# Kernel optimization log

Measured on AMD Instinct MI355X. Metric: run time of the kernel, lower is better.

Reference implementation:

```python
import jax, jax.numpy as jnp
import numpy as np

H, DH, BS = 12, 64, 64          # heads, head_dim, block_size
D, FF, L, EPS = 768, 3072, 12, 1e-12

def _ln(x, g, b):
    m = x.mean(-1, keepdims=True)
    v = ((x - m) ** 2).mean(-1, keepdims=True)
    return (x - m) * jax.lax.rsqrt(v + EPS) * g + b

def setup_inputs() -> dict:
    key = jax.random.key(0)
    ks = iter(jax.random.split(key, 40))
    B, S, IN, C = 2, 4096, 1280, 2
    nb = S // BS
    def p(shape, s=0.02):
        return jax.random.normal(next(ks), shape, jnp.float32) * s
    inp = dict(
        embeddings=jax.random.normal(next(ks), (B, S, IN), jnp.float32),
        attention_mask=jnp.ones((B, S), jnp.int32),
        Wp=p((IN, D)), bp=jnp.zeros((D,), jnp.float32),
        pos_emb=p((S, D)), tok_emb=p((D,)),
        lne_g=jnp.ones((D,), jnp.float32), lne_b=jnp.zeros((D,), jnp.float32),
        Wq=p((L, D, D)), bq=jnp.zeros((L, D), jnp.float32),
        Wk=p((L, D, D)), bk=jnp.zeros((L, D), jnp.float32),
        Wv=p((L, D, D)), bv=jnp.zeros((L, D), jnp.float32),
        Wo=p((L, D, D)), bo=jnp.zeros((L, D), jnp.float32),
        l1g=jnp.ones((L, D), jnp.float32), l1b=jnp.zeros((L, D), jnp.float32),
        W1=p((L, D, FF)), b1=jnp.zeros((L, FF), jnp.float32),
        W2=p((L, FF, D)), b2=jnp.zeros((L, D), jnp.float32),
        l2g=jnp.ones((L, D), jnp.float32), l2b=jnp.zeros((L, D), jnp.float32),
        Wc=p((D, C)), bc=jnp.zeros((C,), jnp.float32),
    )
    # BigBird pattern: each interior query block -> 2 global + 3 window + 3 random key blocks.
    # Random blocks are drawn once (deterministic) like HF's data-independent rand mask.
    rng = np.random.default_rng(0)
    idx, val = [], []
    for i in range(1, nb - 1):
        blocks = [0, nb - 1, i - 1, i, i + 1]
        v = [True, True, i - 1 != 0, True, i + 1 != nb - 1]  # dedupe window/global overlap
        forbid = set(blocks)
        allowed = [x for x in range(nb) if x not in forbid]
        r = rng.choice(allowed, size=3, replace=False).tolist()
        idx.append(blocks + r)
        val.append(v + [True, True, True])
    inp["blk_idx"] = jnp.asarray(np.array(idx, np.int32))    # [nb-2, 8]
    inp["blk_valid"] = jnp.asarray(np.array(val, bool))       # [nb-2, 8]
    return inp

def reference(embeddings, attention_mask, Wp, bp, pos_emb, tok_emb, lne_g, lne_b,
              Wq, bq, Wk, bk, Wv, bv, Wo, bo, l1g, l1b, W1, b1, W2, b2, l2g, l2b,
              Wc, bc, blk_idx, blk_valid):
    B, S, _ = embeddings.shape
    nb = S // BS
    na = blk_idx.shape[1]
    x = embeddings @ Wp + bp + pos_emb + tok_emb
    x = _ln(x, lne_g, lne_b)
    am = attention_mask.astype(jnp.float32)                       # [B,S]
    full_bias = ((am - 1.0) * 1e9)[:, None, None, None, :]        # [B,1,1,1,S]
    amb = am.reshape(B, nb, BS)
    am_g = amb[:, blk_idx].reshape(B, nb - 2, na * BS)            # gathered key mask
    vmask = jnp.repeat(blk_valid, BS, axis=-1)                    # [nb-2, na*BS]
    gb = jnp.where((am_g > 0) & vmask[None], 0.0, -1e9)[:, None, :, None, :]
    scale = 1.0 / np.sqrt(DH).astype(np.float32)

    def layer(x, p):
        wq, bq_, wk, bk_, wv, bv_, wo, bo_, g1, b1_, w1, bi1, w2, bi2, g2, b2_ = p
        q = (x @ wq + bq_).reshape(B, S, H, DH).transpose(0, 2, 1, 3)
        k = (x @ wk + bk_).reshape(B, S, H, DH).transpose(0, 2, 1, 3)
        v = (x @ wv + bv_).reshape(B, S, H, DH).transpose(0, 2, 1, 3)
        qb = q.reshape(B, H, nb, BS, DH)
        kb = k.reshape(B, H, nb, BS, DH)
        vb = v.reshape(B, H, nb, BS, DH)
        # interior query blocks: gather sparse key blocks (global+window+random)
        q_int = qb[:, :, 1:-1]                                     # [B,H,nb-2,BS,DH]
        k_g = kb[:, :, blk_idx].reshape(B, H, nb - 2, na * BS, DH)
        v_g = vb[:, :, blk_idx].reshape(B, H, nb - 2, na * BS, DH)
        s = jnp.einsum('bhiqd,bhikd->bhiqk', q_int, k_g) * scale + gb
        p_ = jax.nn.softmax(s, axis=-1)
        ctx_int = jnp.einsum('bhiqk,bhikd->bhiqd', p_, v_g)
        # first/last blocks are global: attend to all keys
        q_edge = jnp.stack([qb[:, :, 0], qb[:, :, -1]], axis=2)    # [B,H,2,BS,DH]
        se = jnp.einsum('bheqd,bhkd->bheqk', q_edge, k) * scale + full_bias
        pe = jax.nn.softmax(se, axis=-1)
        ctx_e = jnp.einsum('bheqk,bhkd->bheqd', pe, v)
        ctx = jnp.concatenate([ctx_e[:, :, :1], ctx_int, ctx_e[:, :, 1:]], axis=2)
        ctx = ctx.reshape(B, H, S, DH).transpose(0, 2, 1, 3).reshape(B, S, D)
        x = _ln(x + ctx @ wo + bo_, g1, b1_)
        h = jax.nn.gelu(x @ w1 + bi1, approximate=False) @ w2 + bi2
        x = _ln(x + h, g2, b2_)
        return x, None

    x, _ = jax.lax.scan(layer, x, (Wq, bq, Wk, bk, Wv, bv, Wo, bo,
                                   l1g, l1b, W1, b1, W2, b2, l2g, l2b))
    return x[:, 0, :] @ Wc + bc
```

## Files before the change

kernel.cpp:

```cpp
#include <hip/hip_runtime.h>
#include <hip/hip_bf16.h>
#include <math.h>

using bf16 = __hip_bfloat16;
typedef short bf16x8 __attribute__((ext_vector_type(8)));
typedef float f32x4 __attribute__((ext_vector_type(4)));

#define DEV __device__ __forceinline__

constexpr int BATCH = 2, SEQ = 4096, INPD = 1280, DM = 768, FFD = 3072;
constexpr int NL = 12, NH = 12, DHD = 64, NBLK = 64, NCLS = 2;
constexpr int MR = BATCH * SEQ;
constexpr int QKVN = 3 * DM;
constexpr int NJOBS = 62 + 16;
constexpr int PARTF = 64 * 64 + 128;

DEV void gload_lds16(const void* g, void* l) {
  __builtin_amdgcn_global_load_lds(
      (const __attribute__((address_space(1))) unsigned int*)g,
      (__attribute__((address_space(3))) unsigned int*)l, 16, 0, 0);
}

__global__ void k_f32_to_bf16(const float* __restrict__ in, bf16* __restrict__ out, int n) {
  int i = (blockIdx.x * blockDim.x + threadIdx.x) * 4;
  int stride = gridDim.x * blockDim.x * 4;
  for (; i < n; i += stride) {
    float4 v = *(const float4*)(in + i);
    out[i + 0] = __float2bfloat16(v.x);
    out[i + 1] = __float2bfloat16(v.y);
    out[i + 2] = __float2bfloat16(v.z);
    out[i + 3] = __float2bfloat16(v.w);
  }
}

DEV void tr32_tile(const float* __restrict__ src, bf16* __restrict__ dst,
                   int K, int N, int tile, float t[32][33], int tid) {
  int nt = N >> 5;
  int tk = tile / nt, tn = tile - tk * nt;
  int tx = tid & 31, ty = tid >> 5;
#pragma unroll
  for (int i = 0; i < 4; ++i)
    t[ty + 8 * i][tx] = src[(size_t)(tk * 32 + ty + 8 * i) * N + tn * 32 + tx];
  __syncthreads();
#pragma unroll
  for (int i = 0; i < 4; ++i)
    dst[(size_t)(tn * 32 + ty + 8 * i) * K + tk * 32 + tx] = __float2bfloat16(t[tx][ty + 8 * i]);
}

__global__ __launch_bounds__(256) void k_transpose_one(const float* __restrict__ src,
                                                       bf16* __restrict__ dst, int K, int N) {
  __shared__ float t[32][33];
  tr32_tile(src, dst, K, N, blockIdx.x, t, threadIdx.x);
}

__global__ __launch_bounds__(256) void k_transpose_layer(
    const float* __restrict__ Wq, const float* __restrict__ Wk,
    const float* __restrict__ Wv, const float* __restrict__ Wo,
    const float* __restrict__ W1, const float* __restrict__ W2,
    bf16* __restrict__ wqkvT, bf16* __restrict__ woT,
    bf16* __restrict__ w1T, bf16* __restrict__ w2T, int l) {
  __shared__ float t[32][33];
  int id = blockIdx.x;
  const float* src; bf16* dst; int K, N;
  if (id < 1728) {
    int m = id / 576; id -= m * 576;
    src = (m == 0 ? Wq : m == 1 ? Wk : Wv) + (size_t)l * DM * DM;
    dst = wqkvT + (size_t)m * DM * DM; K = DM; N = DM;
  } else if (id < 2304) {
    id -= 1728; src = Wo + (size_t)l * DM * DM; dst = woT; K = DM; N = DM;
  } else if (id < 4608) {
    id -= 2304; src = W1 + (size_t)l * DM * FFD; dst = w1T; K = DM; N = FFD;
  } else {
    id -= 4608; src = W2 + (size_t)l * FFD * DM; dst = w2T; K = FFD; N = DM;
  }
  tr32_tile(src, dst, K, N, id, t, threadIdx.x);
}

template <int EPI>
__global__ __launch_bounds__(256) void k_gemm(
    const bf16* __restrict__ A, const bf16* __restrict__ BT, int N, int K,
    const float* __restrict__ b0, const float* __restrict__ b1, const float* __restrict__ b2,
    const float* __restrict__ res, const float* __restrict__ pos, const float* __restrict__ tok,
    float* __restrict__ Cf, bf16* __restrict__ Cb) {
  __shared__ __align__(16) bf16 lA[128 * 32];
  __shared__ __align__(16) bf16 lB[128 * 32];
  const int tid = threadIdx.x;
  const int bm = blockIdx.y * 128, bn = blockIdx.x * 128;
  const int lane = tid & 63, wid = tid >> 6;
  const int wm = (wid >> 1) * 64, wn = (wid & 1) * 64;
  const int lr = lane & 15, lks = lane >> 4;
  f32x4 acc[4][4] = {};
  for (int k0 = 0; k0 < K; k0 += 32) {
    __syncthreads();
#pragma unroll
    for (int ss = 0; ss < 2; ++ss) {
      int seg = tid + ss * 256;
      int row = seg >> 2, slot = seg & 3;
      int kseg = slot ^ ((row >> 1) & 3);
      gload_lds16(A + (size_t)(bm + row) * K + k0 + kseg * 8, lA + seg * 8);
      gload_lds16(BT + (size_t)(bn + row) * K + k0 + kseg * 8, lB + seg * 8);
    }
    __syncthreads();
    bf16x8 af[4], bfr[4];
#pragma unroll
    for (int m = 0; m < 4; ++m) {
      int r = wm + m * 16 + lr;
      af[m] = *(const bf16x8*)(lA + r * 32 + ((lks ^ ((r >> 1) & 3)) << 3));
    }
#pragma unroll
    for (int n = 0; n < 4; ++n) {
      int r = wn + n * 16 + lr;
      bfr[n] = *(const bf16x8*)(lB + r * 32 + ((lks ^ ((r >> 1) & 3)) << 3));
    }
#pragma unroll
    for (int m = 0; m < 4; ++m)
#pragma unroll
      for (int n = 0; n < 4; ++n)
        acc[m][n] = __builtin_amdgcn_mfma_f32_16x16x32_bf16(af[m], bfr[n], acc[m][n], 0, 0, 0);
  }
  const int gq = lane >> 4;
#pragma unroll
  for (int m = 0; m < 4; ++m) {
#pragma unroll
    for (int n = 0; n < 4; ++n) {
      int gcol = bn + wn + n * 16 + lr;
      f32x4 v = acc[m][n];
#pragma unroll
      for (int r = 0; r < 4; ++r) {
        int grow = bm + wm + m * 16 + gq * 4 + r;
        float x = v[r];
        if constexpr (EPI == 0) {
          int c = gcol; const float* bb = b0;
          if (c >= 2 * DM) { bb = b2; c -= 2 * DM; }
          else if (c >= DM) { bb = b1; c -= DM; }
          x += bb[c];
          Cb[(size_t)grow * N + gcol] = __float2bfloat16(x);
        } else if constexpr (EPI == 1) {
          x += b0[gcol];
          x = 0.5f * x * (1.0f + erff(x * 0.70710678118654752f));
          Cb[(size_t)grow * N + gcol] = __float2bfloat16(x);
        } else if constexpr (EPI == 2) {
          x += b0[gcol] + res[(size_t)grow * N + gcol];
          Cf[(size_t)grow * N + gcol] = x;
        } else {
          x += b0[gcol] + pos[(size_t)(grow & (SEQ - 1)) * N + gcol] + tok[gcol];
          Cf[(size_t)grow * N + gcol] = x;
        }
      }
    }
  }
}

__global__ __launch_bounds__(256) void k_ln(const float* __restrict__ in,
                                            const float* __restrict__ g, const float* __restrict__ b,
                                            float* __restrict__ xf, bf16* __restrict__ xb) {
  const int row = blockIdx.x, tid = threadIdx.x;
  const float* rp = in + (size_t)row * DM;
  float vals[3], s = 0.f, s2 = 0.f;
#pragma unroll
  for (int i = 0; i < 3; ++i) {
    float v = rp[tid + i * 256];
    vals[i] = v; s += v; s2 += v * v;
  }
#pragma unroll
  for (int off = 32; off > 0; off >>= 1) {
    s += __shfl_down(s, off);
    s2 += __shfl_down(s2, off);
  }
  __shared__ float red[8];
  int wv = tid >> 6, lane = tid & 63;
  if (lane == 0) { red[wv] = s; red[4 + wv] = s2; }
  __syncthreads();
  s = red[0] + red[1] + red[2] + red[3];
  s2 = red[4] + red[5] + red[6] + red[7];
  float mean = s * (1.0f / DM);
  float var = s2 * (1.0f / DM) - mean * mean;
  float rs = rsqrtf(var + 1e-12f);
#pragma unroll
  for (int i = 0; i < 3; ++i) {
    int c = tid + i * 256;
    float y = (vals[i] - mean) * rs * g[c] + b[c];
    xf[(size_t)row * DM + c] = y;
    xb[(size_t)row * DM + c] = __float2bfloat16(y);
  }
}

__global__ __launch_bounds__(256) void k_vt(const bf16* __restrict__ qkv, bf16* __restrict__ vt) {
  __shared__ unsigned short t[64][72];
  const int bh = blockIdx.y, t0 = blockIdx.x * 64;
  const int b = bh / NH, h = bh - b * NH;
  const int tid = threadIdx.x;
  const int rr = tid >> 2, cs = (tid & 3) * 16;
  const unsigned short* src = (const unsigned short*)qkv +
      (size_t)(b * SEQ + t0 + rr) * QKVN + 2 * DM + h * DHD + cs;
#pragma unroll
  for (int i = 0; i < 16; ++i) t[cs + i][rr] = src[i];
  __syncthreads();
  unsigned short* dst = (unsigned short*)vt + (size_t)(bh * DHD + rr) * SEQ + t0 + cs;
#pragma unroll
  for (int i = 0; i < 16; ++i) dst[i] = t[rr][cs + i];
}

__global__ __launch_bounds__(256) void k_attn(
    const bf16* __restrict__ qkv, const bf16* __restrict__ vt,
    const int* __restrict__ blk_idx,
    bf16* __restrict__ ctx, float* __restrict__ epart) {
  __shared__ __align__(16) bf16 sQ[64 * 64];
  __shared__ __align__(16) bf16 sK[64 * 64];
  __shared__ __align__(16) bf16 sV[64 * 64];
  __shared__ __align__(16) bf16 sP[4][16 * 64];
  const int job = blockIdx.x;
  const int b = job / (NH * NJOBS);
  const int rem = job - b * NH * NJOBS;
  const int h = rem / NJOBS;
  const int j = rem - h * NJOBS;
  const int tid = threadIdx.x, lane = tid & 63, w = tid >> 6;
  const int lr = lane & 15, lks = lane >> 4;

  const bool interior = (j < 62);
  int qblk, e = 0, split = 0;
  if (interior) qblk = j + 1;
  else { int tt = j - 62; e = tt >> 3; split = tt & 7; qblk = e ? NBLK - 1 : 0; }
  const int qt0 = qblk * 64;

  {
    const bf16* qbase = qkv + (size_t)(b * SEQ + qt0) * QKVN + h * DHD;
#pragma unroll
    for (int ss = 0; ss < 2; ++ss) {
      int seg = tid + ss * 256;
      int row = seg >> 3, slot = seg & 7;
      int kseg = slot ^ (row & 7);
      gload_lds16(qbase + (size_t)row * QKVN + kseg * 8, sQ + seg * 8);
    }
  }
  __syncthreads();
  bf16x8 aq[2];
#pragma unroll
  for (int kk = 0; kk < 2; ++kk) {
    int rq = w * 16 + lr;
    int slot = (kk * 4 + lks) ^ (rq & 7);
    aq[kk] = *(const bf16x8*)(sQ + rq * 64 + slot * 8);
  }

  float m_r[4], l_r[4];
  f32x4 o[4] = {};
#pragma unroll
  for (int r = 0; r < 4; ++r) { m_r[r] = -1e30f; l_r[r] = 0.f; }

  for (int kb = 0; kb < 8; ++kb) {
    int kbi;
    if (interior) {
      if ((j == 0 && kb == 2) || (j == 61 && kb == 4)) continue;
      kbi = blk_idx[j * 8 + kb];
    } else {
      kbi = split * 8 + kb;
    }
    const int kt0 = kbi * 64;
    __syncthreads();
    {
      const bf16* kbase = qkv + (size_t)(b * SEQ + kt0) * QKVN + DM + h * DHD;
      const bf16* vbase = vt + (size_t)((b * NH + h) * DHD) * SEQ + kt0;
#pragma unroll
      for (int ss = 0; ss < 2; ++ss) {
        int seg = tid + ss * 256;
        int row = seg >> 3, slot = seg & 7;
        int kseg = slot ^ (row & 7);
        gload_lds16(kbase + (size_t)row * QKVN + kseg * 8, sK + seg * 8);
        gload_lds16(vbase + (size_t)row * SEQ + kseg * 8, sV + seg * 8);
      }
    }
    __syncthreads();
    f32x4 sfr[4];
#pragma unroll
    for (int n = 0; n < 4; ++n) {
      f32x4 z = {};
#pragma unroll
      for (int kk = 0; kk < 2; ++kk) {
        int rk = n * 16 + lr;
        int slot = (kk * 4 + lks) ^ (rk & 7);
        bf16x8 kf = *(const bf16x8*)(sK + rk * 64 + slot * 8);
        z = __builtin_amdgcn_mfma_f32_16x16x32_bf16(aq[kk], kf, z, 0, 0, 0);
      }
      sfr[n] = z;
    }
#pragma unroll
    for (int n = 0; n < 4; ++n)
#pragma unroll
      for (int r = 0; r < 4; ++r) sfr[n][r] *= 0.125f;
    float alpha[4];
#pragma unroll
    for (int r = 0; r < 4; ++r) {
      float tmx = fmaxf(fmaxf(sfr[0][r], sfr[1][r]), fmaxf(sfr[2][r], sfr[3][r]));
#pragma unroll
      for (int off = 1; off < 16; off <<= 1) tmx = fmaxf(tmx, __shfl_xor(tmx, off));
      float mnew = fmaxf(m_r[r], tmx);
      alpha[r] = __expf(m_r[r] - mnew);
      m_r[r] = mnew;
    }
#pragma unroll
    for (int r = 0; r < 4; ++r) {
      float su = 0.f;
#pragma unroll
      for (int n = 0; n < 4; ++n) {
        float p = __expf(sfr[n][r] - m_r[r]);
        sfr[n][r] = p;
        su += p;
      }
#pragma unroll
      for (int off = 1; off < 16; off <<= 1) su += __shfl_xor(su, off);
      l_r[r] = l_r[r] * alpha[r] + su;
    }
#pragma unroll
    for (int n = 0; n < 4; ++n) {
#pragma unroll
      for (int r = 0; r < 4; ++r) {
        int prow = lks * 4 + r;
        int col = n * 16 + lr;
        int eo = prow * 64 + ((((col >> 3) ^ (prow & 7)) << 3) | (col & 7));
        sP[w][eo] = __float2bfloat16(sfr[n][r]);
      }
    }
#pragma unroll
    for (int n = 0; n < 4; ++n)
#pragma unroll
      for (int r = 0; r < 4; ++r) o[n][r] *= alpha[r];
    asm volatile("s_waitcnt lgkmcnt(0)" ::: "memory");
    bf16x8 pa[2];
#pragma unroll
    for (int kk = 0; kk < 2; ++kk) {
      int slot = (kk * 4 + lks) ^ (lr & 7);
      pa[kk] = *(const bf16x8*)(sP[w] + lr * 64 + slot * 8);
    }
#pragma unroll
    for (int n = 0; n < 4; ++n) {
#pragma unroll
      for (int kk = 0; kk < 2; ++kk) {
        int rv = n * 16 + lr;
        int slot = (kk * 4 + lks) ^ (rv & 7);
        bf16x8 vf = *(const bf16x8*)(sV + rv * 64 + slot * 8);
        o[n] = __builtin_amdgcn_mfma_f32_16x16x32_bf16(pa[kk], vf, o[n], 0, 0, 0);
      }
    }
  }
  if (interior) {
#pragma unroll
    for (int r = 0; r < 4; ++r) {
      float inv = 1.0f / l_r[r];
      int tok = qt0 + w * 16 + lks * 4 + r;
#pragma unroll
      for (int n = 0; n < 4; ++n) {
        int col = h * DHD + n * 16 + lr;
        ctx[(size_t)(b * SEQ + tok) * DM + col] = __float2bfloat16(o[n][r] * inv);
      }
    }
  } else {
    float* base = epart + (size_t)((((b * NH + h) * 2 + e) * 8) + split) * PARTF;
#pragma unroll
    for (int r = 0; r < 4; ++r) {
      int qrow = w * 16 + lks * 4 + r;
#pragma unroll
      for (int n = 0; n < 4; ++n)
        base[qrow * 64 + n * 16 + lr] = o[n][r];
      if (lr == 0) { base[4096 + qrow] = m_r[r]; base[4096 + 64 + qrow] = l_r[r]; }
    }
  }
}

__global__ __launch_bounds__(256) void k_combine(const float* __restrict__ epart,
                                                 bf16* __restrict__ ctx) {
  const int bid = blockIdx.x;
  const int b = bid / (NH * 2);
  const int rem = bid - b * NH * 2;
  const int h = rem >> 1, e = rem & 1;
  const int tid = threadIdx.x;
  const int row = tid >> 2, cq = tid & 3;
  const float* base0 = epart + (size_t)(((b * NH + h) * 2 + e) * 8) * PARTF;
  float ms[8], ls[8], M = -1e30f;
#pragma unroll
  for (int s = 0; s < 8; ++s) {
    const float* bp = base0 + (size_t)s * PARTF;
    ms[s] = bp[4096 + row];
    ls[s] = bp[4096 + 64 + row];
    M = fmaxf(M, ms[s]);
  }
  float Lt = 0.f, accv[16];
#pragma unroll
  for (int i = 0; i < 16; ++i) accv[i] = 0.f;
#pragma unroll
  for (int s = 0; s < 8; ++s) {
    float wgt = __expf(ms[s] - M);
    Lt += ls[s] * wgt;
    const float* op = base0 + (size_t)s * PARTF + row * 64 + cq * 16;
#pragma unroll
    for (int i = 0; i < 16; ++i) accv[i] += op[i] * wgt;
  }
  float inv = 1.0f / Lt;
  int qblk = e ? NBLK - 1 : 0;
  int tok = qblk * 64 + row;
  bf16* cp = ctx + (size_t)(b * SEQ + tok) * DM + h * DHD + cq * 16;
#pragma unroll
  for (int i = 0; i < 16; ++i) cp[i] = __float2bfloat16(accv[i] * inv);
}

__global__ void k_classifier(const float* __restrict__ xf, const float* __restrict__ Wc,
                             const float* __restrict__ bc, float* __restrict__ out) {
  const int tid = threadIdx.x, lane = tid & 63, wv = tid >> 6;
  const int b = wv >> 1, c = wv & 1;
  float s = 0.f;
  for (int d = lane; d < DM; d += 64)
    s += xf[(size_t)(b * SEQ) * DM + d] * Wc[d * NCLS + c];
#pragma unroll
  for (int off = 32; off > 0; off >>= 1) s += __shfl_down(s, off);
  if (lane == 0) out[b * NCLS + c] = s + bc[c];
}

extern "C" void kernel_launch(void* const* d_in, const int* in_sizes, int n_in,
                              void* d_out, int out_size, void* d_ws, size_t ws_size,
                              hipStream_t stream) {
  const float* embeddings = (const float*)d_in[0];
  const float* Wp  = (const float*)d_in[2];
  const float* bp  = (const float*)d_in[3];
  const float* pos = (const float*)d_in[4];
  const float* tokv = (const float*)d_in[5];
  const float* lng = (const float*)d_in[6];
  const float* lnb = (const float*)d_in[7];
  const float* Wq  = (const float*)d_in[8];
  const float* bq  = (const float*)d_in[9];
  const float* Wk  = (const float*)d_in[10];
  const float* bk  = (const float*)d_in[11];
  const float* Wv  = (const float*)d_in[12];
  const float* bv  = (const float*)d_in[13];
  const float* Wo  = (const float*)d_in[14];
  const float* bo  = (const float*)d_in[15];
  const float* l1g = (const float*)d_in[16];
  const float* l1b = (const float*)d_in[17];
  const float* W1  = (const float*)d_in[18];
  const float* b1  = (const float*)d_in[19];
  const float* W2  = (const float*)d_in[20];
  const float* b2  = (const float*)d_in[21];
  const float* l2g = (const float*)d_in[22];
  const float* l2b = (const float*)d_in[23];
  const float* Wc  = (const float*)d_in[24];
  const float* bc  = (const float*)d_in[25];
  const int*  bidx = (const int*)d_in[26];
  (void)in_sizes; (void)n_in; (void)out_size; (void)ws_size;

  char* ws = (char*)d_ws;
  size_t off = 0;
  auto alloc = [&](size_t bytes) -> char* {
    char* p = ws + off;
    off += (bytes + 255) & ~(size_t)255;
    return p;
  };
  bf16*  embB  = (bf16*)alloc((size_t)MR * INPD * 2);
  bf16*  wpT   = (bf16*)alloc((size_t)DM * INPD * 2);
  bf16*  wqkvT = (bf16*)alloc((size_t)QKVN * DM * 2);
  bf16*  woT   = (bf16*)alloc((size_t)DM * DM * 2);
  bf16*  w1T   = (bf16*)alloc((size_t)FFD * DM * 2);
  bf16*  w2T   = (bf16*)alloc((size_t)DM * FFD * 2);
  float* xf    = (float*)alloc((size_t)MR * DM * 4);
  bf16*  xb    = (bf16*)alloc((size_t)MR * DM * 2);
  float* preLN = (float*)alloc((size_t)MR * DM * 4);
  bf16*  qkvB  = (bf16*)alloc((size_t)MR * QKVN * 2);
  bf16*  vtB   = (bf16*)alloc((size_t)BATCH * NH * DHD * SEQ * 2);
  bf16*  ctxB  = (bf16*)alloc((size_t)MR * DM * 2);
  bf16*  hB    = (bf16*)alloc((size_t)MR * FFD * 2);
  float* epart = (float*)alloc((size_t)BATCH * NH * 2 * 8 * PARTF * 4);

  k_f32_to_bf16<<<2048, 256, 0, stream>>>(embeddings, embB, MR * INPD);
  k_transpose_one<<<(INPD / 32) * (DM / 32), 256, 0, stream>>>(Wp, wpT, INPD, DM);
  k_gemm<3><<<dim3(DM / 128, MR / 128), 256, 0, stream>>>(embB, wpT, DM, INPD,
      bp, nullptr, nullptr, nullptr, pos, tokv, preLN, nullptr);
  k_ln<<<MR, 256, 0, stream>>>(preLN, lng, lnb, xf, xb);

  for (int l = 0; l < NL; ++l) {
    k_transpose_layer<<<6912, 256, 0, stream>>>(Wq, Wk, Wv, Wo, W1, W2,
        wqkvT, woT, w1T, w2T, l);
    k_gemm<0><<<dim3(QKVN / 128, MR / 128), 256, 0, stream>>>(xb, wqkvT, QKVN, DM,
        bq + (size_t)l * DM, bk + (size_t)l * DM, bv + (size_t)l * DM,
        nullptr, nullptr, nullptr, nullptr, qkvB);
    k_vt<<<dim3(SEQ / 64, BATCH * NH), 256, 0, stream>>>(qkvB, vtB);
    k_attn<<<BATCH * NH * NJOBS, 256, 0, stream>>>(qkvB, vtB, bidx, ctxB, epart);
    k_combine<<<BATCH * NH * 2, 256, 0, stream>>>(epart, ctxB);
    k_gemm<2><<<dim3(DM / 128, MR / 128), 256, 0, stream>>>(ctxB, woT, DM, DM,
        bo + (size_t)l * DM, nullptr, nullptr, xf, nullptr, nullptr, preLN, nullptr);
    k_ln<<<MR, 256, 0, stream>>>(preLN, l1g + (size_t)l * DM, l1b + (size_t)l * DM, xf, xb);
    k_gemm<1><<<dim3(FFD / 128, MR / 128), 256, 0, stream>>>(xb, w1T, FFD, DM,
        b1 + (size_t)l * FFD, nullptr, nullptr, nullptr, nullptr, nullptr, nullptr, hB);
    k_gemm<2><<<dim3(DM / 128, MR / 128), 256, 0, stream>>>(hB, w2T, DM, FFD,
        b2 + (size_t)l * DM, nullptr, nullptr, xf, nullptr, nullptr, preLN, nullptr);
    k_ln<<<MR, 256, 0, stream>>>(preLN, l2g + (size_t)l * DM, l2b + (size_t)l * DM, xf, xb);
  }
  k_classifier<<<1, 256, 0, stream>>>(xf, Wc, bc, (float*)d_out);
}
```

Measured before the change: 3.994 ms.

## Double-buffer GEMM LDS tiles and remap workgroups for XCD locality

The GEMM kernel now keeps two LDS buffers and issues the next k-tile's global-to-LDS loads before running MFMAs on the current tile, with one barrier per iteration instead of two. It also remaps the linear workgroup id so each of the 8 XCDs processes a contiguous range of output tiles, aiming to improve L2 reuse of shared A/B panels. LDS usage doubles, which may reduce occupancy. Correctness relies on the barrier also waiting for the async LDS loads.

Result: faster. 3.713 ms (-7.0%).

```diff
diff --git a/kernel.cpp b/kernel.cpp
--- a/kernel.cpp
+++ b/kernel.cpp
@@ -82,41 +82,59 @@
     const float* __restrict__ b0, const float* __restrict__ b1, const float* __restrict__ b2,
     const float* __restrict__ res, const float* __restrict__ pos, const float* __restrict__ tok,
     float* __restrict__ Cf, bf16* __restrict__ Cb) {
-  __shared__ __align__(16) bf16 lA[128 * 32];
-  __shared__ __align__(16) bf16 lB[128 * 32];
+  __shared__ __align__(16) bf16 lA[2][128 * 32];
+  __shared__ __align__(16) bf16 lB[2][128 * 32];
   const int tid = threadIdx.x;
-  const int bm = blockIdx.y * 128, bn = blockIdx.x * 128;
+  const int gx = gridDim.x;
+  const int nwg = gx * gridDim.y;
+  const int orig = blockIdx.y * gx + blockIdx.x;
+  const int q = nwg >> 3, r = nwg & 7;
+  const int xcd = orig & 7, pos_ = orig >> 3;
+  const int tile = (xcd < r ? xcd * (q + 1) : r * (q + 1) + (xcd - r) * q) + pos_;
+  const int bx = tile % gx, by = tile / gx;
+  const int bm = by * 128, bn = bx * 128;
   const int lane = tid & 63, wid = tid >> 6;
   const int wm = (wid >> 1) * 64, wn = (wid & 1) * 64;
   const int lr = lane & 15, lks = lane >> 4;
-  f32x4 acc[4][4] = {};
-  for (int k0 = 0; k0 < K; k0 += 32) {
-    __syncthreads();
+  const bf16* Abase = A + (size_t)bm * K;
+  const bf16* Bbase = BT + (size_t)bn * K;
+
+  auto stage = [&](int buf, int t) {
+    int k0 = t << 5;
 #pragma unroll
     for (int ss = 0; ss < 2; ++ss) {
       int seg = tid + ss * 256;
       int row = seg >> 2, slot = seg & 3;
       int kseg = slot ^ ((row >> 1) & 3);
-      gload_lds16(A + (size_t)(bm + row) * K + k0 + kseg * 8, lA + seg * 8);
-      gload_lds16(BT + (size_t)(bn + row) * K + k0 + kseg * 8, lB + seg * 8);
-    }
-    __syncthreads();
+      gload_lds16(Abase + (size_t)row * K + k0 + kseg * 8, &lA[buf][seg * 8]);
+      gload_lds16(Bbase + (size_t)row * K + k0 + kseg * 8, &lB[buf][seg * 8]);
+    }
+  };
+
+  f32x4 acc[4][4] = {};
+  const int nt = K >> 5;
+  stage(0, 0);
+  __syncthreads();
+  for (int t = 0; t < nt; ++t) {
+    const int buf = t & 1;
+    if (t + 1 < nt) stage(buf ^ 1, t + 1);
     bf16x8 af[4], bfr[4];
 #pragma unroll
     for (int m = 0; m < 4; ++m) {
-      int r = wm + m * 16 + lr;
-      af[m] = *(const bf16x8*)(lA + r * 32 + ((lks ^ ((r >> 1) & 3)) << 3));
+      int rr = wm + m * 16 + lr;
+      af[m] = *(const bf16x8*)(&lA[buf][rr * 32 + ((lks ^ ((rr >> 1) & 3)) << 3)]);
     }
 #pragma unroll
     for (int n = 0; n < 4; ++n) {
-      int r = wn + n * 16 + lr;
-      bfr[n] = *(const bf16x8*)(lB + r * 32 + ((lks ^ ((r >> 1) & 3)) << 3));
+      int rr = wn + n * 16 + lr;
+      bfr[n] = *(const bf16x8*)(&lB[buf][rr * 32 + ((lks ^ ((rr >> 1) & 3)) << 3)]);
     }
 #pragma unroll
     for (int m = 0; m < 4; ++m)
 #pragma unroll
       for (int n = 0; n < 4; ++n)
         acc[m][n] = __builtin_amdgcn_mfma_f32_16x16x32_bf16(af[m], bfr[n], acc[m][n], 0, 0, 0);
+    __syncthreads();
   }
   const int gq = lane >> 4;
 #pragma unroll
@@ -126,9 +144,9 @@
       int gcol = bn + wn + n * 16 + lr;
       f32x4 v = acc[m][n];
 #pragma unroll
-      for (int r = 0; r < 4; ++r) {
-        int grow = bm + wm + m * 16 + gq * 4 + r;
-        float x = v[r];
+      for (int rr = 0; rr < 4; ++rr) {
+        int grow = bm + wm + m * 16 + gq * 4 + rr;
+        float x = v[rr];
         if constexpr (EPI == 0) {
           int c = gcol; const float* bb = b0;
           if (c >= 2 * DM) { bb = b2; c -= 2 * DM; }
```
